# Performance work log

Hardware: AMD Instinct MI355X
Metric: run time of the kernel (lower is better)

The kernel has to match this reference:

```python
import math
import jax, jax.numpy as jnp
import numpy as np

H, PQ, PV = 12, 8, 12
C_S = 384
INF, EPS = 1e5, 1e-8
SOFTPLUS_INV_1 = 0.541324854612918


def _rand_rot(key, shape):
    """Random rotation matrices via normalized quaternions, shape + (3,3)."""
    q = jax.random.normal(key, shape + (4,))
    q = q / jnp.linalg.norm(q, axis=-1, keepdims=True)
    w, x, y, z = q[..., 0], q[..., 1], q[..., 2], q[..., 3]
    R = jnp.stack([
        1 - 2 * (y * y + z * z), 2 * (x * y - w * z), 2 * (x * z + w * y),
        2 * (x * y + w * z), 1 - 2 * (x * x + z * z), 2 * (y * z - w * x),
        2 * (x * z - w * y), 2 * (y * z + w * x), 1 - 2 * (x * x + y * y),
    ], axis=-1).reshape(shape + (3, 3))
    return R


def setup_inputs() -> dict:
    key = jax.random.key(0)
    ks = jax.random.split(key, 12)
    B, N1, N2 = 2, 2048, 512
    s1 = jax.random.normal(ks[0], (B, N1, C_S), dtype=jnp.float32)
    s2 = jax.random.normal(ks[1], (B, N2, C_S), dtype=jnp.float32)
    r1_rot = _rand_rot(ks[2], (B, N1)).astype(jnp.float32)
    r2_rot = _rand_rot(ks[3], (B, N2)).astype(jnp.float32)
    r1_trans = jax.random.normal(ks[4], (B, N1, 3), dtype=jnp.float32)
    r2_trans = jax.random.normal(ks[5], (B, N2, 3), dtype=jnp.float32)
    mask1 = jnp.ones((B, N1), dtype=jnp.float32)
    mask2 = jnp.ones((B, N2), dtype=jnp.float32)
    Wq = jax.random.normal(ks[6], (C_S, H * PQ * 3), dtype=jnp.float32) / math.sqrt(C_S)
    Wkv = jax.random.normal(ks[7], (C_S, H * (PQ + PV) * 3), dtype=jnp.float32) / math.sqrt(C_S)
    head_weights = jnp.full((H,), SOFTPLUS_INV_1, dtype=jnp.float32)
    Wout = jax.random.normal(ks[8], (H * PV * 4, C_S), dtype=jnp.float32) * 0.02
    bout = jnp.zeros((C_S,), dtype=jnp.float32)
    return {"s1": s1, "s2": s2, "r1_rot": r1_rot, "r1_trans": r1_trans,
            "r2_rot": r2_rot, "r2_trans": r2_trans, "mask1": mask1, "mask2": mask2,
            "Wq": Wq, "Wkv": Wkv, "head_weights": head_weights,
            "Wout": Wout, "bout": bout}


def reference(s1, s2, r1_rot, r1_trans, r2_rot, r2_trans, mask1, mask2,
              Wq, Wkv, head_weights, Wout, bout):
    B, N1, _ = s1.shape
    N2 = s2.shape[1]

    # query points: linear -> [B,N1,3,H,PQ] (torch split/stack layout) -> local [B,N1,H,PQ,3]
    q = jnp.moveaxis((s1 @ Wq).reshape(B, N1, 3, H, PQ), 2, -1)
    # rigid apply: R x + t (global frame)
    q = jnp.einsum('bimn,bihpn->bihpm', r1_rot, q) + r1_trans[:, :, None, None, :]

    kv = jnp.moveaxis((s2 @ Wkv).reshape(B, N2, 3, H, PQ + PV), 2, -1)
    kv = jnp.einsum('bjmn,bjhpn->bjhpm', r2_rot, kv) + r2_trans[:, :, None, None, :]
    k, v = kv[..., :PQ, :], kv[..., PQ:, :]  # [B,N2,H,PQ,3], [B,N2,H,PV,3]

    # sum_p ||q_p - k_p||^2 via norm expansion (avoids [B,N1,N2,H,PQ,3] tensor)
    qn = jnp.sum(q * q, axis=(-1, -2))                     # [B,N1,H]
    kn = jnp.sum(k * k, axis=(-1, -2))                     # [B,N2,H]
    cross = jnp.einsum('bihpc,bjhpc->bijh', q, k)          # [B,N1,N2,H]
    d2 = qn[:, :, None, :] + kn[:, None, :, :] - 2.0 * cross

    hw = jax.nn.softplus(head_weights) * math.sqrt(1.0 / (3 * (PQ * 9.0 / 2)))
    att = jnp.transpose(-0.5 * d2 * hw, (0, 3, 1, 2))      # [B,H,N1,N2]
    bias = INF * (mask1[:, :, None] * mask2[:, None, :] - 1.0)
    a = jax.nn.softmax(att + bias[:, None], axis=-1)

    o = jnp.einsum('bhij,bjhpc->bihpc', a, v)              # [B,N1,H,PV,3]
    # rigid invert_apply: R^T (x - t), back into local frame of residue i
    o_loc = jnp.einsum('bimn,bihpm->bihpn', r1_rot, o - r1_trans[:, :, None, None, :])

    dists = jnp.sqrt(jnp.sum(o_loc * o_loc, axis=-1) + EPS)   # [B,N1,H,PV]
    o_flat = o_loc.reshape(B, N1, H * PV, 3)
    feats = jnp.concatenate([o_flat[..., 0], o_flat[..., 1], o_flat[..., 2],
                             dists.reshape(B, N1, H * PV)], axis=-1)
    return feats @ Wout + bout
```

## Files before the change

kernel.cpp:

```cpp
#include <hip/hip_runtime.h>
#include <math.h>

#define B_ 2
#define N1_ 2048
#define N2_ 512
#define CS_ 384
#define H_ 12
#define PQ_ 8
#define PV_ 12
#define PKV_ 20
#define CQ_ (H_*PQ_*3)
#define CKV_ (H_*PKV_*3)
#define INF_ 100000.0f
#define HW_SCALE_ 0.09622504486493764f
#define LOG2E_ 1.4426950408889634f

typedef __attribute__((ext_vector_type(8))) short bf16x8;
typedef __attribute__((ext_vector_type(4))) float f32x4;

__device__ inline unsigned short f2bf(float x) {
  unsigned u = __float_as_uint(x);
  u += 0x7fffu + ((u >> 16) & 1u);
  return (unsigned short)(u >> 16);
}

__device__ inline bf16x8 cvt8(const float* __restrict__ p) {
  float4 a = *(const float4*)p;
  float4 b = *(const float4*)(p + 4);
  bf16x8 r;
  r[0] = (short)f2bf(a.x); r[1] = (short)f2bf(a.y);
  r[2] = (short)f2bf(a.z); r[3] = (short)f2bf(a.w);
  r[4] = (short)f2bf(b.x); r[5] = (short)f2bf(b.y);
  r[6] = (short)f2bf(b.z); r[7] = (short)f2bf(b.w);
  return r;
}

#define TQ_   108
#define TKV_  276
#define TWO_  216
#define VPAD_ 72
#define KN_   12
#define S1B_  768
#define S2B_  192
#define PREP_GRID_ (TQ_+TKV_+TWO_+VPAD_+KN_+S1B_+S2B_)
__global__ __launch_bounds__(256) void prep_kernel(
    const float* __restrict__ Wq, const float* __restrict__ Wkv,
    const float* __restrict__ Wout,
    const float* __restrict__ s1, const float* __restrict__ s2,
    unsigned short* __restrict__ wqT, unsigned short* __restrict__ wkvT,
    unsigned short* __restrict__ woutT,
    unsigned short* __restrict__ vtb, float* __restrict__ kn,
    unsigned short* __restrict__ s1b, unsigned short* __restrict__ s2b)
{
  __shared__ float lds[32][33];
  int blk = blockIdx.x, t = threadIdx.x;
  int rr0 = t >> 5, cc = t & 31;

  const float* src = nullptr; unsigned short* dst = nullptr;
  int K = 0, N = 0, k0 = 0, n0 = 0;
  if (blk < TQ_) {
    src = Wq; dst = wqT; K = 384; N = CQ_;
    k0 = (blk % 12) * 32; n0 = (blk / 12) * 32;
  } else if (blk < TQ_ + TKV_) {
    int b2 = blk - TQ_;
    src = Wkv; dst = wkvT; K = 384; N = CKV_;
    k0 = (b2 % 12) * 32; n0 = (b2 / 12) * 32;
  } else if (blk < TQ_ + TKV_ + TWO_) {
    int b3 = blk - TQ_ - TKV_;
    src = Wout; dst = woutT; K = 576; N = CS_;
    k0 = (b3 % 18) * 32; n0 = (b3 / 18) * 32;
  } else if (blk < TQ_ + TKV_ + TWO_ + VPAD_) {
    int idx = (blk - TQ_ - TKV_ - TWO_)*256 + t;
    int f = idx * 8;
    int run = f >> 9, off = f & 511;
    int bh = run / 12, cc2 = 36 + run % 12;
    uint4 z = {0u,0u,0u,0u};
    *(uint4*)(vtb + ((size_t)bh*48 + cc2)*512 + off) = z;
    return;
  } else if (blk < TQ_ + TKV_ + TWO_ + VPAD_ + KN_) {
    int idx = (blk - TQ_ - TKV_ - TWO_ - VPAD_)*256 + t;
    float4 z = {0.f,0.f,0.f,0.f};
    *(float4*)(kn + (size_t)idx*4) = z;
    return;
  } else if (blk < TQ_ + TKV_ + TWO_ + VPAD_ + KN_ + S1B_) {
    size_t idx = (size_t)(blk - TQ_ - TKV_ - TWO_ - VPAD_ - KN_)*256 + t;
    *(bf16x8*)(s1b + idx*8) = cvt8(s1 + idx*8);
    return;
  } else {
    size_t idx = (size_t)(blk - TQ_ - TKV_ - TWO_ - VPAD_ - KN_ - S1B_)*256 + t;
    *(bf16x8*)(s2b + idx*8) = cvt8(s2 + idx*8);
    return;
  }

  #pragma unroll
  for (int rr = 0; rr < 4; ++rr) {
    int r = rr0 + rr*8;
    if (n0 + cc < N) lds[r][cc] = src[(size_t)(k0 + r)*N + n0 + cc];
  }
  __syncthreads();
  #pragma unroll
  for (int rr = 0; rr < 4; ++rr) {
    int r = rr0 + rr*8;
    if (n0 + r < N) dst[(size_t)(n0 + r)*K + k0 + cc] = f2bf(lds[cc][r]);
  }
}

__global__ __launch_bounds__(512) void proj_mfma(
    const unsigned short* __restrict__ s1b, const unsigned short* __restrict__ s2b,
    const unsigned short* __restrict__ wqT, const unsigned short* __restrict__ wkvT,
    const float* __restrict__ r1_rot, const float* __restrict__ r1_trans,
    const float* __restrict__ r2_rot, const float* __restrict__ r2_trans,
    unsigned short* __restrict__ qgb, float* __restrict__ qn,
    unsigned short* __restrict__ kgb, unsigned short* __restrict__ vtb,
    float* __restrict__ kn)
{
  __shared__ float merge_s[4][64][13];
  int wave = threadIdx.x >> 6, lane = threadIdx.x & 63;
  int col = lane & 15, g = lane >> 4;
  int pr = wave >> 1, kh = wave & 1;
  int k0 = kh * 192;

  if (blockIdx.x < 384) {
    int pid = blockIdx.x*4 + pr;
    int strip = pid / 6;
    int nt = pid % 6;
    int i0 = strip * 16;

    f32x4 ax = {0.f,0.f,0.f,0.f}, ay = ax, az = ax;
    const unsigned short* arow = s1b + (size_t)(i0 + col)*CS_ + k0;
    const unsigned short* bx = wqT + (size_t)((nt     )*16 + col)*CS_ + k0;
    const unsigned short* by = wqT + (size_t)((nt +  6)*16 + col)*CS_ + k0;
    const unsigned short* bz = wqT + (size_t)((nt + 12)*16 + col)*CS_ + k0;
    #pragma unroll
    for (int k = 0; k < 192; k += 32) {
      bf16x8 a = *(const bf16x8*)(arow + k + g*8);
      ax = __builtin_amdgcn_mfma_f32_16x16x32_bf16(a, *(const bf16x8*)(bx + k + g*8), ax, 0,0,0);
      ay = __builtin_amdgcn_mfma_f32_16x16x32_bf16(a, *(const bf16x8*)(by + k + g*8), ay, 0,0,0);
      az = __builtin_amdgcn_mfma_f32_16x16x32_bf16(a, *(const bf16x8*)(bz + k + g*8), az, 0,0,0);
    }
    if (kh) {
      #pragma unroll
      for (int r = 0; r < 4; ++r) {
        merge_s[pr][lane][r]     = ax[r];
        merge_s[pr][lane][4 + r] = ay[r];
        merge_s[pr][lane][8 + r] = az[r];
      }
    }
    __syncthreads();
    if (kh) return;
    #pragma unroll
    for (int r = 0; r < 4; ++r) {
      ax[r] += merge_s[pr][lane][r];
      ay[r] += merge_s[pr][lane][4 + r];
      az[r] += merge_s[pr][lane][8 + r];
    }

    int p = nt*16 + col;
    int h = p >> 3, pq = p & 7;
    float qsum[4];
    #pragma unroll
    for (int r = 0; r < 4; ++r) {
      int row = i0 + g*4 + r;
      const float* R  = r1_rot   + (size_t)row*9;
      const float* tr = r1_trans + (size_t)row*3;
      float x = ax[r], y = ay[r], z = az[r];
      float g0 = R[0]*x + R[1]*y + R[2]*z + tr[0];
      float g1 = R[3]*x + R[4]*y + R[5]*z + tr[1];
      float g2 = R[6]*x + R[7]*y + R[8]*z + tr[2];
      int b = row >> 11, i = row & (N1_-1);
      size_t rbase = ((size_t)(b*H_ + h)*N1_ + i)*32;
      qgb[rbase + pq*3]     = f2bf(g0);
      qgb[rbase + pq*3 + 1] = f2bf(g1);
      qgb[rbase + pq*3 + 2] = f2bf(g2);
      if (pq == 7) {
        uint4 z4 = {0u,0u,0u,0u};
        *(uint4*)(qgb + rbase + 24) = z4;
      }
      qsum[r] = g0*g0 + g1*g1 + g2*g2;
    }
    #pragma unroll
    for (int r = 0; r < 4; ++r) {
      qsum[r] += __shfl_xor(qsum[r], 1);
      qsum[r] += __shfl_xor(qsum[r], 2);
      qsum[r] += __shfl_xor(qsum[r], 4);
    }
    if ((col & 7) == 0) {
      int hh = nt*2 + (col >> 3);
      #pragma unroll
      for (int r = 0; r < 4; ++r) {
        int row = i0 + g*4 + r;
        int b = row >> 11, i = row & (N1_-1);
        qn[(size_t)(b*H_ + hh)*N1_ + i] = qsum[r];
      }
    }
  } else {
    int pid = (blockIdx.x - 384)*4 + pr;
    int strip = pid / 15;
    int nt = pid % 15;
    int row0 = strip * 16;

    f32x4 ax = {0.f,0.f,0.f,0.f}, ay = ax, az = ax;
    const unsigned short* arow = s2b + (size_t)(row0 + col)*CS_ + k0;
    const unsigned short* bx = wkvT + (size_t)(nt*16       + col)*CS_ + k0;
    const unsigned short* by = wkvT + (size_t)(nt*16 + 240 + col)*CS_ + k0;
    const unsigned short* bz = wkvT + (size_t)(nt*16 + 480 + col)*CS_ + k0;
    #pragma unroll
    for (int k = 0; k < 192; k += 32) {
      bf16x8 a = *(const bf16x8*)(arow + k + g*8);
      ax = __builtin_amdgcn_mfma_f32_16x16x32_bf16(a, *(const bf16x8*)(bx + k + g*8), ax, 0,0,0);
      ay = __builtin_amdgcn_mfma_f32_16x16x32_bf16(a, *(const bf16x8*)(by + k + g*8), ay, 0,0,0);
      az = __builtin_amdgcn_mfma_f32_16x16x32_bf16(a, *(const bf16x8*)(bz + k + g*8), az, 0,0,0);
    }
    if (kh) {
      #pragma unroll
      for (int r = 0; r < 4; ++r) {
        merge_s[pr][lane][r]     = ax[r];
        merge_s[pr][lane][4 + r] = ay[r];
        merge_s[pr][lane][8 + r] = az[r];
      }
    }
    __syncthreads();
    if (kh) return;
    #pragma unroll
    for (int r = 0; r < 4; ++r) {
      ax[r] += merge_s[pr][lane][r];
      ay[r] += merge_s[pr][lane][4 + r];
      az[r] += merge_s[pr][lane][8 + r];
    }

    int p = nt*16 + col;
    int h = p / PKV_, pp = p % PKV_;
    #pragma unroll
    for (int r = 0; r < 4; ++r) {
      int row = row0 + g*4 + r;
      const float* R  = r2_rot   + (size_t)row*9;
      const float* tr = r2_trans + (size_t)row*3;
      float x = ax[r], y = ay[r], z = az[r];
      float g0 = R[0]*x + R[1]*y + R[2]*z + tr[0];
      float g1 = R[3]*x + R[4]*y + R[5]*z + tr[1];
      float g2 = R[6]*x + R[7]*y + R[8]*z + tr[2];
      int b = row >> 9, j = row & (N2_-1);
      int bh = b*H_ + h;
      if (pp < PQ_) {
        size_t base = ((size_t)bh*N2_ + j)*32 + pp*3;
        kgb[base]   = f2bf(g0);
        kgb[base+1] = f2bf(g1);
        kgb[base+2] = f2bf(g2);
        if (pp == 0) {
          uint4 z4 = {0u,0u,0u,0u};
          *(uint4*)(kgb + ((size_t)bh*N2_ + j)*32 + 24) = z4;
        }
        atomicAdd(&kn[(size_t)bh*N2_ + j], g0*g0 + g1*g1 + g2*g2);
      } else {
        int comp = (pp - PQ_)*3;
        size_t base = ((size_t)bh*48 + comp)*512 + j;
        vtb[base]        = f2bf(g0);
        vtb[base + 512]  = f2bf(g1);
        vtb[base + 1024] = f2bf(g2);
      }
    }
  }
}

#define RSTRIDE 72
#define OSTRIDE 51
#define WSLOT 3328
#define FSTRIDE 584
__global__ __launch_bounds__(768, 6) void attn_fused(
    const unsigned short* __restrict__ qgb, const float* __restrict__ qn,
    const unsigned short* __restrict__ kgb, const unsigned short* __restrict__ vtb,
    const float* __restrict__ kn, const float* __restrict__ mask1,
    const float* __restrict__ mask2, const float* __restrict__ hwts,
    const float* __restrict__ rot, const float* __restrict__ trans,
    const unsigned short* __restrict__ woutT, const float* __restrict__ bout,
    float* __restrict__ out)
{
  __shared__ __align__(16) unsigned char ovl[12*WSLOT];
  __shared__ __align__(16) unsigned short feats_s[8][FSTRIDE];
  __shared__ float l_s[12][16];

  int wave = threadIdx.x >> 6;
  int lane = threadIdx.x & 63;
  int col = lane & 15, g = lane >> 4;
  int b = blockIdx.x >> 8;
  int it8 = blockIdx.x & 255;
  int i0 = it8 * 8;
  int h = wave;
  int bh = b*H_ + h;

  unsigned short* ps = (unsigned short*)(ovl + wave*WSLOT);
  float*          os = (float*)(ovl + wave*WSLOT);

  float hw   = logf(1.0f + __expf(hwts[h])) * HW_SCALE_;
  float hwl  = hw * LOG2E_;
  float mneg = -INF_ * LOG2E_;

  bf16x8 qa = *(const bf16x8*)(qgb + (((size_t)bh*N1_ + i0 + (col & 7))*32 + g*8));

  float ar[4], m1l[4];
  #pragma unroll
  for (int r = 0; r < 4; ++r) {
    int ig = i0 + ((g*4 + r) & 7);
    ar[r]  = -0.5f*hwl * qn[(size_t)bh*N1_ + ig];
    m1l[r] = mask1[b*N1_ + ig] * (INF_*LOG2E_);
  }

  f32x4 ot[3];
  #pragma unroll
  for (int m = 0; m < 3; ++m) ot[m] = (f32x4){0.f,0.f,0.f,0.f};
  float l[4] = {0.f,0.f,0.f,0.f};

  const unsigned short* kbase = kgb + (size_t)bh*N2_*32;
  const unsigned short* vbase = vtb + (size_t)bh*48*512;
  const float* knp = kn + (size_t)bh*N2_;
  const float* m2p = mask2 + b*N2_;

  for (int jt = 0; jt < 8; ++jt) {
    int j0 = jt*64;
    #pragma unroll
    for (int nt = 0; nt < 4; ++nt) {
      int jg = j0 + nt*16 + col;
      bf16x8 kb = *(const bf16x8*)(kbase + ((size_t)jg*32 + g*8));
      f32x4 dotv = __builtin_amdgcn_mfma_f32_16x16x32_bf16(
          qa, kb, (f32x4){0.f,0.f,0.f,0.f}, 0, 0, 0);
      float bc  = -0.5f*hwl*knp[jg];
      float m2c = m2p[jg];
      #pragma unroll
      for (int r = 0; r < 4; ++r) {
        float logit = fmaf(hwl, dotv[r], fmaf(m1l[r], m2c, mneg) + (ar[r] + bc));
        float w = __builtin_amdgcn_exp2f(logit);
        l[r] += w;
        ps[(g*4 + r)*RSTRIDE + nt*16 + col] = f2bf(w);
      }
    }
    #pragma unroll
    for (int ks = 0; ks < 2; ++ks) {
      bf16x8 pb = *(const bf16x8*)&ps[col*RSTRIDE + ks*32 + g*8];
      #pragma unroll
      for (int mtv = 0; mtv < 3; ++mtv) {
        bf16x8 va = *(const bf16x8*)(vbase +
            ((size_t)(mtv*16 + col))*512 + j0 + ks*32 + g*8);
        ot[mtv] = __builtin_amdgcn_mfma_f32_16x16x32_bf16(va, pb, ot[mtv], 0, 0, 0);
      }
    }
  }

  #pragma unroll
  for (int r = 0; r < 4; ++r) {
    l[r] += __shfl_xor(l[r], 1);
    l[r] += __shfl_xor(l[r], 2);
    l[r] += __shfl_xor(l[r], 4);
    l[r] += __shfl_xor(l[r], 8);
  }
  __builtin_amdgcn_sched_barrier(0);
  if (col == 0) {
    #pragma unroll
    for (int r = 0; r < 4; ++r) l_s[wave][g*4 + r] = l[r];
  }
  #pragma unroll
  for (int mtv = 0; mtv < 3; ++mtv)
    #pragma unroll
    for (int r = 0; r < 4; ++r)
      os[col*OSTRIDE + mtv*16 + g*4 + r] = ot[mtv][r];
  __syncthreads();

  if (col < 8) {
    float inv = 1.0f / l_s[wave][col];
    int row = b*N1_ + i0 + col;
    const float* R  = rot   + (size_t)row*9;
    const float* tr = trans + (size_t)row*3;
    float R00=R[0],R01=R[1],R02=R[2],R10=R[3],R11=R[4],R12=R[5],R20=R[6],R21=R[7],R22=R[8];
    float t0=tr[0], t1=tr[1], t2=tr[2];
    int h12 = h*PV_;
    #pragma unroll
    for (int p = 0; p < 3; ++p) {
      int pt = g*3 + p;
      float ox = os[col*OSTRIDE + pt*3+0]*inv - t0;
      float oy = os[col*OSTRIDE + pt*3+1]*inv - t1;
      float oz = os[col*OSTRIDE + pt*3+2]*inv - t2;
      float lx = R00*ox + R10*oy + R20*oz;
      float ly = R01*ox + R11*oy + R21*oz;
      float lz = R02*ox + R12*oy + R22*oz;
      float dist = sqrtf(lx*lx + ly*ly + lz*lz + 1e-8f);
      feats_s[col][      h12 + pt] = f2bf(lx);
      feats_s[col][144 + h12 + pt] = f2bf(ly);
      feats_s[col][288 + h12 + pt] = f2bf(lz);
      feats_s[col][432 + h12 + pt] = f2bf(dist);
    }
  }
  __syncthreads();

  {
    int n0 = wave * 32;
    f32x4 acc0 = {0.f,0.f,0.f,0.f}, acc1 = acc0;
    const unsigned short* b0 = woutT + (size_t)(n0      + col)*576;
    const unsigned short* b1 = woutT + (size_t)(n0 + 16 + col)*576;
    #pragma unroll 3
    for (int k = 0; k < 576; k += 32) {
      bf16x8 a = *(const bf16x8*)&feats_s[col & 7][k + g*8];
      acc0 = __builtin_amdgcn_mfma_f32_16x16x32_bf16(a, *(const bf16x8*)(b0 + k + g*8), acc0, 0,0,0);
      acc1 = __builtin_amdgcn_mfma_f32_16x16x32_bf16(a, *(const bf16x8*)(b1 + k + g*8), acc1, 0,0,0);
    }
    if (g < 2) {
      int rowbase = b*N1_ + i0;
      float bb0 = bout[n0 + col];
      float bb1 = bout[n0 + 16 + col];
      #pragma unroll
      for (int r = 0; r < 4; ++r) {
        size_t orow = (size_t)(rowbase + g*4 + r)*CS_;
        out[orow + n0 + col]      = acc0[r] + bb0;
        out[orow + n0 + 16 + col] = acc1[r] + bb1;
      }
    }
  }
}

extern "C" void kernel_launch(void* const* d_in, const int* in_sizes, int n_in,
                              void* d_out, int out_size, void* d_ws, size_t ws_size,
                              hipStream_t stream) {
  const float* s1       = (const float*)d_in[0];
  const float* s2       = (const float*)d_in[1];
  const float* r1_rot   = (const float*)d_in[2];
  const float* r1_trans = (const float*)d_in[3];
  const float* r2_rot   = (const float*)d_in[4];
  const float* r2_trans = (const float*)d_in[5];
  const float* mask1    = (const float*)d_in[6];
  const float* mask2    = (const float*)d_in[7];
  const float* Wq       = (const float*)d_in[8];
  const float* Wkv      = (const float*)d_in[9];
  const float* hwts     = (const float*)d_in[10];
  const float* Wout     = (const float*)d_in[11];
  const float* bout     = (const float*)d_in[12];
  float* out = (float*)d_out;

  float* qn = (float*)d_ws;
  float* kn = qn + (size_t)B_*H_*N1_;
  unsigned short* qgb  = (unsigned short*)(kn + (size_t)B_*H_*N2_);
  unsigned short* kgb  = qgb  + (size_t)B_*H_*N1_*32;
  unsigned short* vtb  = kgb  + (size_t)B_*H_*N2_*32;
  unsigned short* wqT  = vtb  + (size_t)B_*H_*48*512;
  unsigned short* wkvT = wqT  + (size_t)CQ_*CS_;
  unsigned short* woutT= wkvT + (size_t)CKV_*CS_;
  unsigned short* s1b  = woutT+ (size_t)CS_*576;
  unsigned short* s2b  = s1b  + (size_t)B_*N1_*CS_;

  prep_kernel<<<PREP_GRID_, 256, 0, stream>>>(
      Wq, Wkv, Wout, s1, s2, wqT, wkvT, woutT, vtb, kn, s1b, s2b);
  proj_mfma<<<624, 512, 0, stream>>>(s1b, s2b, wqT, wkvT, r1_rot, r1_trans,
                                     r2_rot, r2_trans, qgb, qn, kgb, vtb, kn);
  attn_fused<<<B_*(N1_/8), 768, 0, stream>>>(qgb, qn, kgb, vtb, kn, mask1, mask2,
                                             hwts, r1_rot, r1_trans, woutT, bout, out);
}
```

Baseline: 179.8 us.

## Process 16 query rows per block with swapped MFMA operands and packed bf16 stores

Each attention block now handles 16 query rows instead of 8. Before, half of each 16-wide MFMA tile was wasted because the query rows were duplicated, and the grid was twice as large. The QK MFMA operands are swapped so each lane holds four consecutive keys, which lets k-norm and mask2 load as float4 and P be written as packed bf16 pairs via v_cvt_pk_bf16_f32 into a repacked LDS layout. The row-sum reduction drops to two shuffles, s_setprio raises priority around the PV MFMAs, and the launch-bounds occupancy hint falls from 6 to 3. The risks are lower occupancy and more work per block across only 256 blocks.

```diff
diff --git a/kernel.cpp b/kernel.cpp
--- a/kernel.cpp
+++ b/kernel.cpp
@@ -17,11 +17,18 @@
 
 typedef __attribute__((ext_vector_type(8))) short bf16x8;
 typedef __attribute__((ext_vector_type(4))) float f32x4;
+typedef __attribute__((ext_vector_type(4))) unsigned int u32x4;
 
 __device__ inline unsigned short f2bf(float x) {
   unsigned u = __float_as_uint(x);
   u += 0x7fffu + ((u >> 16) & 1u);
   return (unsigned short)(u >> 16);
+}
+
+__device__ inline unsigned cvtpk_bf16(float lo, float hi) {
+  unsigned d;
+  asm("v_cvt_pk_bf16_f32 %0, %1, %2" : "=v"(d) : "v"(lo), "v"(hi));
+  return d;
 }
 
 __device__ inline bf16x8 cvt8(const float* __restrict__ p) {
@@ -262,11 +269,10 @@
   }
 }
 
-#define RSTRIDE 72
 #define OSTRIDE 51
-#define WSLOT 3328
+#define WSLOT 3264
 #define FSTRIDE 584
-__global__ __launch_bounds__(768, 6) void attn_fused(
+__global__ __launch_bounds__(768, 3) void attn_fused(
     const unsigned short* __restrict__ qgb, const float* __restrict__ qn,
     const unsigned short* __restrict__ kgb, const unsigned short* __restrict__ vtb,
     const float* __restrict__ kn, const float* __restrict__ mask1,
@@ -276,87 +282,88 @@
     float* __restrict__ out)
 {
   __shared__ __align__(16) unsigned char ovl[12*WSLOT];
-  __shared__ __align__(16) unsigned short feats_s[8][FSTRIDE];
+  __shared__ __align__(16) unsigned short feats_s[16][FSTRIDE];
   __shared__ float l_s[12][16];
 
   int wave = threadIdx.x >> 6;
   int lane = threadIdx.x & 63;
   int col = lane & 15, g = lane >> 4;
-  int b = blockIdx.x >> 8;
-  int it8 = blockIdx.x & 255;
-  int i0 = it8 * 8;
+  int b = blockIdx.x >> 7;
+  int it = blockIdx.x & 127;
   int h = wave;
   int bh = b*H_ + h;
 
-  unsigned short* ps = (unsigned short*)(ovl + wave*WSLOT);
-  float*          os = (float*)(ovl + wave*WSLOT);
+  unsigned* pw = (unsigned*)(ovl + wave*WSLOT);
+  float*    os = (float*)(ovl + wave*WSLOT);
 
   float hw   = logf(1.0f + __expf(hwts[h])) * HW_SCALE_;
   float hwl  = hw * LOG2E_;
+  float nh   = -0.5f * hwl;
   float mneg = -INF_ * LOG2E_;
 
-  bf16x8 qa = *(const bf16x8*)(qgb + (((size_t)bh*N1_ + i0 + (col & 7))*32 + g*8));
-
-  float ar[4], m1l[4];
-  #pragma unroll
-  for (int r = 0; r < 4; ++r) {
-    int ig = i0 + ((g*4 + r) & 7);
-    ar[r]  = -0.5f*hwl * qn[(size_t)bh*N1_ + ig];
-    m1l[r] = mask1[b*N1_ + ig] * (INF_*LOG2E_);
-  }
+  bf16x8 qa = *(const bf16x8*)(qgb + (((size_t)bh*N1_ + it*16 + col)*32 + g*8));
+
+  int ig = it*16 + col;
+  float ar  = nh * qn[(size_t)bh*N1_ + ig];
+  float m1l = mask1[b*N1_ + ig] * (INF_*LOG2E_);
+  float arm = ar + mneg;
 
   f32x4 ot[3];
   #pragma unroll
   for (int m = 0; m < 3; ++m) ot[m] = (f32x4){0.f,0.f,0.f,0.f};
-  float l[4] = {0.f,0.f,0.f,0.f};
-
-  const unsigned short* kbase = kgb + (size_t)bh*N2_*32;
-  const unsigned short* vbase = vtb + (size_t)bh*48*512;
-  const float* knp = kn + (size_t)bh*N2_;
-  const float* m2p = mask2 + b*N2_;
+  float l = 0.f;
+
+  const unsigned short* kptr = kgb + (size_t)bh*N2_*32 + col*32 + g*8;
+  const unsigned short* vp0 = vtb + (size_t)bh*48*512 + (size_t)(     col)*512 + g*8;
+  const unsigned short* vp1 = vtb + (size_t)bh*48*512 + (size_t)(16 + col)*512 + g*8;
+  const unsigned short* vp2 = vtb + (size_t)bh*48*512 + (size_t)(32 + col)*512 + g*8;
+  const float* knp = kn + (size_t)bh*N2_ + g*4;
+  const float* m2p = mask2 + b*N2_ + g*4;
+
+  int wslot = (col*4 + g)*9;
+  int rbase = (col*4 + ((g&1)<<1))*9 + ((g>>1)<<1);
 
   for (int jt = 0; jt < 8; ++jt) {
-    int j0 = jt*64;
     #pragma unroll
     for (int nt = 0; nt < 4; ++nt) {
-      int jg = j0 + nt*16 + col;
-      bf16x8 kb = *(const bf16x8*)(kbase + ((size_t)jg*32 + g*8));
+      bf16x8 kb = *(const bf16x8*)(kptr + nt*512);
       f32x4 dotv = __builtin_amdgcn_mfma_f32_16x16x32_bf16(
-          qa, kb, (f32x4){0.f,0.f,0.f,0.f}, 0, 0, 0);
-      float bc  = -0.5f*hwl*knp[jg];
-      float m2c = m2p[jg];
+          kb, qa, (f32x4){0.f,0.f,0.f,0.f}, 0, 0, 0);
+      float4 knv = *(const float4*)(knp + nt*16);
+      float4 m2v = *(const float4*)(m2p + nt*16);
+      float w[4];
       #pragma unroll
       for (int r = 0; r < 4; ++r) {
-        float logit = fmaf(hwl, dotv[r], fmaf(m1l[r], m2c, mneg) + (ar[r] + bc));
-        float w = __builtin_amdgcn_exp2f(logit);
-        l[r] += w;
-        ps[(g*4 + r)*RSTRIDE + nt*16 + col] = f2bf(w);
-      }
-    }
+        float t = fmaf(m1l, ((const float*)&m2v)[r], arm);
+        t = fmaf(nh, ((const float*)&knv)[r], t);
+        t = fmaf(hwl, dotv[r], t);
+        w[r] = __builtin_amdgcn_exp2f(t);
+        l += w[r];
+      }
+      pw[wslot + nt*2]     = cvtpk_bf16(w[0], w[1]);
+      pw[wslot + nt*2 + 1] = cvtpk_bf16(w[2], w[3]);
+    }
+    __builtin_amdgcn_s_setprio(1);
     #pragma unroll
     for (int ks = 0; ks < 2; ++ks) {
-      bf16x8 pb = *(const bf16x8*)&ps[col*RSTRIDE + ks*32 + g*8];
-      #pragma unroll
-      for (int mtv = 0; mtv < 3; ++mtv) {
-        bf16x8 va = *(const bf16x8*)(vbase +
-            ((size_t)(mtv*16 + col))*512 + j0 + ks*32 + g*8);
-        ot[mtv] = __builtin_amdgcn_mfma_f32_16x16x32_bf16(va, pb, ot[mtv], 0, 0, 0);
-      }
-    }
-  }
-
-  #pragma unroll
-  for (int r = 0; r < 4; ++r) {
-    l[r] += __shfl_xor(l[r], 1);
-    l[r] += __shfl_xor(l[r], 2);
-    l[r] += __shfl_xor(l[r], 4);
-    l[r] += __shfl_xor(l[r], 8);
-  }
+      u32x4 pd;
+      pd[0] = pw[rbase + ks*4];
+      pd[1] = pw[rbase + ks*4 + 1];
+      pd[2] = pw[rbase + 9 + ks*4];
+      pd[3] = pw[rbase + 9 + ks*4 + 1];
+      bf16x8 pb = *(bf16x8*)&pd;
+      ot[0] = __builtin_amdgcn_mfma_f32_16x16x32_bf16(*(const bf16x8*)(vp0 + ks*32), pb, ot[0], 0,0,0);
+      ot[1] = __builtin_amdgcn_mfma_f32_16x16x32_bf16(*(const bf16x8*)(vp1 + ks*32), pb, ot[1], 0,0,0);
+      ot[2] = __builtin_amdgcn_mfma_f32_16x16x32_bf16(*(const bf16x8*)(vp2 + ks*32), pb, ot[2], 0,0,0);
+    }
+    __builtin_amdgcn_s_setprio(0);
+    kptr += 2048; vp0 += 64; vp1 += 64; vp2 += 64; knp += 64; m2p += 64;
+  }
+
+  l += __shfl_xor(l, 16);
+  l += __shfl_xor(l, 32);
   __builtin_amdgcn_sched_barrier(0);
-  if (col == 0) {
-    #pragma unroll
-    for (int r = 0; r < 4; ++r) l_s[wave][g*4 + r] = l[r];
-  }
+  if (g == 0) l_s[wave][col] = l;
   #pragma unroll
   for (int mtv = 0; mtv < 3; ++mtv)
     #pragma unroll
@@ -364,9 +371,9 @@
       os[col*OSTRIDE + mtv*16 + g*4 + r] = ot[mtv][r];
   __syncthreads();
 
-  if (col < 8) {
+  {
     float inv = 1.0f / l_s[wave][col];
-    int row = b*N1_ + i0 + col;
+    int row = b*N1_ + it*16 + col;
     const float* R  = rot   + (size_t)row*9;
     const float* tr = trans + (size_t)row*3;
     float R00=R[0],R01=R[1],R02=R[2],R10=R[3],R11=R[4],R12=R[5],R20=R[6],R21=R[7],R22=R[8];
@@ -397,20 +404,18 @@
     const unsigned short* b1 = woutT + (size_t)(n0 + 16 + col)*576;
     #pragma unroll 3
     for (int k = 0; k < 576; k += 32) {
-      bf16x8 a = *(const bf16x8*)&feats_s[col & 7][k + g*8];
+      bf16x8 a = *(const bf16x8*)&feats_s[col][k + g*8];
       acc0 = __builtin_amdgcn_mfma_f32_16x16x32_bf16(a, *(const bf16x8*)(b0 + k + g*8), acc0, 0,0,0);
       acc1 = __builtin_amdgcn_mfma_f32_16x16x32_bf16(a, *(const bf16x8*)(b1 + k + g*8), acc1, 0,0,0);
     }
-    if (g < 2) {
-      int rowbase = b*N1_ + i0;
-      float bb0 = bout[n0 + col];
-      float bb1 = bout[n0 + 16 + col];
-      #pragma unroll
-      for (int r = 0; r < 4; ++r) {
-        size_t orow = (size_t)(rowbase + g*4 + r)*CS_;
-        out[orow + n0 + col]      = acc0[r] + bb0;
-        out[orow + n0 + 16 + col] = acc1[r] + bb1;
-      }
+    int rowbase = b*N1_ + it*16;
+    float bb0 = bout[n0 + col];
+    float bb1 = bout[n0 + 16 + col];
+    #pragma unroll
+    for (int r = 0; r < 4; ++r) {
+      size_t orow = (size_t)(rowbase + g*4 + r)*CS_;
+      out[orow + n0 + col]      = acc0[r] + bb0;
+      out[orow + n0 + 16 + col] = acc1[r] + bb1;
     }
   }
 }
@@ -448,6 +453,6 @@
       Wq, Wkv, Wout, s1, s2, wqT, wkvT, woutT, vtb, kn, s1b, s2b);
   proj_mfma<<<624, 512, 0, stream>>>(s1b, s2b, wqT, wkvT, r1_rot, r1_trans,
                                      r2_rot, r2_trans, qgb, qn, kgb, vtb, kn);
-  attn_fused<<<B_*(N1_/8), 768, 0, stream>>>(qgb, qn, kgb, vtb, kn, mask1, mask2,
-                                             hwts, r1_rot, r1_trans, woutT, bout, out);
-}
+  attn_fused<<<B_*(N1_/16), 768, 0, stream>>>(qgb, qn, kgb, vtb, kn, mask1, mask2,
+                                              hwts, r1_rot, r1_trans, woutT, bout, out);
+}
```

Measured after the change: 151.1 us. -16.0%, faster.
